# Optimization experiments

Hardware: AMD Instinct MI355X
Metric: run time of the kernel (lower is better)

Reference implementation:

```python
import jax, jax.numpy as jnp
import numpy as np

N = 100000   # nodes
E = 1600000  # edges (avg degree 16)
D = 256      # in_channels == dim (forward hard-codes BatchNorm1d(256))
BN_EPS = 1e-5


def _batchnorm(x, gamma, beta):
    # training-mode BatchNorm1d: batch statistics over node dim, biased variance
    mu = jnp.mean(x, axis=0)
    var = jnp.var(x, axis=0)
    return (x - mu) * jax.lax.rsqrt(var + BN_EPS) * gamma + beta


def _gin_conv(x, src, dst, n, W1, b1, gamma, beta, W2, b2):
    # GINConv, eps=0: nn((1+eps)*x + sum_{j in N(i)} x_j)
    agg = jax.ops.segment_sum(x[src], dst, num_segments=n)  # sparse neighbor sum
    h = x + agg
    h = jax.nn.relu(_batchnorm(h @ W1 + b1, gamma, beta))
    return jax.nn.relu(h @ W2 + b2)


def setup_inputs() -> dict:
    key = jax.random.key(0)
    ks = jax.random.split(key, 8)
    x = jax.random.normal(ks[0], (N, D), dtype=jnp.float32)
    edge_index = jax.random.randint(ks[1], (2, E), 0, N, dtype=jnp.int64)
    s = 0.02
    inp = {
        "x": x,
        "edge_index": edge_index,
        # fresh BatchNorm1d(256) in forward (default affine params)
        "g0": jnp.ones((D,), jnp.float32),
        "b0": jnp.zeros((D,), jnp.float32),
        # conv1 MLP: Linear-BN-ReLU-Linear-ReLU
        "W1a": jax.random.normal(ks[2], (D, D), jnp.float32) * s,
        "b1a": jnp.zeros((D,), jnp.float32),
        "g1": jnp.ones((D,), jnp.float32),
        "bt1": jnp.zeros((D,), jnp.float32),
        "W1b": jax.random.normal(ks[3], (D, D), jnp.float32) * s,
        "b1b": jnp.zeros((D,), jnp.float32),
        # conv2 MLP
        "W2a": jax.random.normal(ks[4], (D, D), jnp.float32) * s,
        "b2a": jnp.zeros((D,), jnp.float32),
        "g2": jnp.ones((D,), jnp.float32),
        "bt2": jnp.zeros((D,), jnp.float32),
        "W2b": jax.random.normal(ks[5], (D, D), jnp.float32) * s,
        "b2b": jnp.zeros((D,), jnp.float32),
    }
    return inp


def reference(x, edge_index, g0, b0, W1a, b1a, g1, bt1, W1b, b1b,
              W2a, b2a, g2, bt2, W2b, b2b):
    n = x.shape[0]
    src, dst = edge_index[0], edge_index[1]
    h = _batchnorm(x, g0, b0)                       # fresh BN(256) on input
    h = _gin_conv(h, src, dst, n, W1a, b1a, g1, bt1, W1b, b1b)
    h = jax.nn.relu(h)                              # outer relu (dropout=eval, identity)
    h = _gin_conv(h, src, dst, n, W2a, b2a, g2, bt2, W2b, b2b)
    return jax.nn.relu(h)
```

## Files before the change

kernel.cpp:

```cpp
#include <hip/hip_runtime.h>

#define N_NODES 100000
#define N_EDGES 1600000
#define DIM 256

typedef unsigned short bf16u;
typedef __attribute__((ext_vector_type(8))) short bf16x8s;
typedef __attribute__((ext_vector_type(4))) float f32x4;

__device__ __forceinline__ float bf2f(unsigned int u16) {
    union { unsigned int i; float f; } x; x.i = u16 << 16; return x.f;
}
__device__ __forceinline__ bf16u f2bf(float f) {
    union { float f; unsigned int i; } x; x.f = f;
    unsigned int i = x.i;
    return (bf16u)((i + 0x7fffu + ((i >> 16) & 1u)) >> 16);
}
__device__ __forceinline__ float loadv(const void* p, size_t i, int isf32) {
    return isf32 ? ((const float*)p)[i] : bf2f(((const bf16u*)p)[i]);
}
__device__ __forceinline__ void async_copy16(const void* g, void* l) {
    __builtin_amdgcn_global_load_lds((const __attribute__((address_space(1))) void*)g,
                                     (__attribute__((address_space(3))) void*)l, 16, 0, 0);
}

__global__ void zero_ints(int* p, int n) {
    int i = blockIdx.x * 256 + threadIdx.x;
    if (i < n) p[i] = 0;
}
__global__ void zero_floats(float* p, int n) {
    int i = blockIdx.x * 256 + threadIdx.x;
    if (i < n) p[i] = 0.f;
}

__global__ void detect_flags(const unsigned* xw, const int* ei, int* flags) {
    __shared__ int cnt, nz;
    if (threadIdx.x == 0) { cnt = 0; nz = 0; }
    __syncthreads();
    unsigned u = xw[threadIdx.x];
    float av = fabsf(bf2f(u & 0xffffu));
    if (av > 1e-5f && av < 50.f) atomicAdd(&cnt, 1);
    if (ei[2 * threadIdx.x + 1] != 0) atomicAdd(&nz, 1);
    __syncthreads();
    if (threadIdx.x == 0) {
        flags[0] = (cnt >= 128) ? 0 : 1;
        if (nz == 0) { flags[1] = 2; flags[2] = 2 * N_EDGES; }
        else         { flags[1] = 1; flags[2] = N_EDGES; }
    }
}

__global__ void transpose_w(const void* W0, const void* W1, const void* W2, const void* W3,
                            bf16u* Wt, const int* flags) {
    __shared__ bf16u tile[64][65];
    int isf32 = flags[0];
    const void* W = (blockIdx.y == 0) ? W0 : (blockIdx.y == 1) ? W1 : (blockIdx.y == 2) ? W2 : W3;
    bf16u* out = Wt + (size_t)blockIdx.y * DIM * DIM;
    int t = threadIdx.x;
    int tx = t & 63, ty = t >> 6;
    int k0 = (blockIdx.x >> 2) * 64, n0 = (blockIdx.x & 3) * 64;
#pragma unroll
    for (int i = 0; i < 16; ++i) {
        int r = ty + i * 4;
        tile[tx][r] = f2bf(loadv(W, (size_t)(k0 + r) * DIM + (n0 + tx), isf32));
    }
    __syncthreads();
#pragma unroll
    for (int i = 0; i < 16; ++i) {
        int r = ty + i * 4;
        out[(size_t)(n0 + r) * DIM + (k0 + tx)] = tile[r][tx];
    }
}

__global__ void col_stats(const void* X, int nrows, float* sums, const int* flags, int dual) {
    __shared__ float ls[512];
    int isf32 = dual ? flags[0] : 0;
    int t = threadIdx.x;
    ls[t] = 0.f; ls[t + 256] = 0.f;
    __syncthreads();
    int rpb = (nrows + gridDim.x - 1) / gridDim.x;
    int r0 = blockIdx.x * rpb;
    int r1 = r0 + rpb; if (r1 > nrows) r1 = nrows;
    int cg = (t & 31) * 8;
    float s[8], q[8];
#pragma unroll
    for (int j = 0; j < 8; ++j) { s[j] = 0.f; q[j] = 0.f; }
    for (int r = r0 + (t >> 5); r < r1; r += 8) {
        size_t base = (size_t)r * DIM + cg;
#pragma unroll
        for (int j = 0; j < 8; ++j) {
            float f = loadv(X, base + j, isf32);
            s[j] += f; q[j] += f * f;
        }
    }
#pragma unroll
    for (int j = 0; j < 8; ++j) {
        atomicAdd(&ls[cg + j], s[j]);
        atomicAdd(&ls[256 + cg + j], q[j]);
    }
    __syncthreads();
    atomicAdd(&sums[t], ls[t]);
    atomicAdd(&sums[256 + t], ls[256 + t]);
}

__global__ void bn_finalize(const float* sums, const void* gamma, const void* beta,
                            float* sc, float* sh, float inv_n, const int* flags) {
    int isf32 = flags[0];
    int t = threadIdx.x;
    float mu = sums[t] * inv_n;
    float var = sums[256 + t] * inv_n - mu * mu;
    float rs = rsqrtf(var + 1e-5f);
    float g = loadv(gamma, t, isf32), b = loadv(beta, t, isf32);
    sc[t] = rs * g;
    sh[t] = b - mu * rs * g;
}

__global__ void bn_apply(const void* X, const float* sc, const float* sh, bf16u* Y,
                         const int* flags, int dual, int relu) {
    int isf32 = dual ? flags[0] : 0;
    size_t i = (size_t)blockIdx.x * 256 + threadIdx.x;
    int c = ((int)(i & 31)) * 8;
    size_t base = i * 8;
    float v[8];
    if (isf32) {
        f32x4 x0 = *(const f32x4*)((const float*)X + base);
        f32x4 x1 = *(const f32x4*)((const float*)X + base + 4);
#pragma unroll
        for (int j = 0; j < 4; ++j) { v[j] = x0[j]; v[4 + j] = x1[j]; }
    } else {
        uint4 u = *(const uint4*)((const bf16u*)X + base);
        v[0] = bf2f(u.x & 0xffffu); v[1] = bf2f(u.x >> 16);
        v[2] = bf2f(u.y & 0xffffu); v[3] = bf2f(u.y >> 16);
        v[4] = bf2f(u.z & 0xffffu); v[5] = bf2f(u.z >> 16);
        v[6] = bf2f(u.w & 0xffffu); v[7] = bf2f(u.w >> 16);
    }
    f32x4 s0 = *(const f32x4*)(sc + c), s1 = *(const f32x4*)(sc + c + 4);
    f32x4 h0 = *(const f32x4*)(sh + c), h1 = *(const f32x4*)(sh + c + 4);
    float y[8];
#pragma unroll
    for (int j = 0; j < 4; ++j) {
        y[j]     = v[j]     * s0[j] + h0[j];
        y[4 + j] = v[4 + j] * s1[j] + h1[j];
    }
    if (relu) {
#pragma unroll
        for (int j = 0; j < 8; ++j) y[j] = fmaxf(y[j], 0.f);
    }
    uint4 ov;
    ov.x = (unsigned)f2bf(y[0]) | ((unsigned)f2bf(y[1]) << 16);
    ov.y = (unsigned)f2bf(y[2]) | ((unsigned)f2bf(y[3]) << 16);
    ov.z = (unsigned)f2bf(y[4]) | ((unsigned)f2bf(y[5]) << 16);
    ov.w = (unsigned)f2bf(y[6]) | ((unsigned)f2bf(y[7]) << 16);
    *(uint4*)(Y + base) = ov;
}

__global__ void edge_hist(const int* ei, const int* flags, int* deg) {
    int e = blockIdx.x * 256 + threadIdx.x;
    if (e < N_EDGES) atomicAdd(&deg[ei[(size_t)flags[2] + (size_t)e * flags[1]]], 1);
}

__global__ void scan1(const int* deg, int* rp, int* bsum) {
    __shared__ int s[256];
    int t = threadIdx.x;
    int i = blockIdx.x * 256 + t;
    s[t] = (i < N_NODES) ? deg[i] : 0;
    __syncthreads();
    for (int off = 1; off < 256; off <<= 1) {
        int nv = (t >= off) ? s[t - off] : 0;
        __syncthreads();
        s[t] += nv;
        __syncthreads();
    }
    if (i < N_NODES) rp[i + 1] = s[t];
    if (t == 255) bsum[blockIdx.x] = s[255];
}

__global__ void scan2(int* bsum, int nblocks) {
    __shared__ int s[512];
    int t = threadIdx.x;
    s[t] = (t < nblocks) ? bsum[t] : 0;
    __syncthreads();
    for (int off = 1; off < 512; off <<= 1) {
        int nv = (t >= off) ? s[t - off] : 0;
        __syncthreads();
        s[t] += nv;
        __syncthreads();
    }
    if (t < nblocks) bsum[t] = s[t];
}

__global__ void scan3(int* rp, const int* bsum) {
    int i = blockIdx.x * 256 + threadIdx.x;
    if (i == 0) rp[0] = 0;
    if (i < N_NODES) {
        int b = i >> 8;
        if (b > 0) rp[i + 1] += bsum[b - 1];
    }
}

__global__ void csr_fill(const int* ei, const int* flags, const int* rp, int* fill, int* col) {
    int e = blockIdx.x * 256 + threadIdx.x;
    if (e < N_EDGES) {
        int d = ei[(size_t)flags[2] + (size_t)e * flags[1]];
        int s = ei[(size_t)e * flags[1]];
        int p = rp[d] + atomicAdd(&fill[d], 1);
        col[p] = s;
    }
}

__global__ void aggregate(const bf16u* h, const int* rp, const int* col, bf16u* out) {
    int node = blockIdx.x * 4 + (threadIdx.x >> 6);
    int lane = threadIdx.x & 63;
    const uint2* hv = (const uint2*)h;
    uint2 u = hv[(size_t)node * 64 + lane];
    float a0 = bf2f(u.x & 0xffffu), a1 = bf2f(u.x >> 16);
    float a2 = bf2f(u.y & 0xffffu), a3 = bf2f(u.y >> 16);
    float b0 = 0.f, b1 = 0.f, b2 = 0.f, b3 = 0.f;
    float c0 = 0.f, c1 = 0.f, c2 = 0.f, c3 = 0.f;
    float d0 = 0.f, d1 = 0.f, d2 = 0.f, d3 = 0.f;
    int e = rp[node], e1 = rp[node + 1];
    for (; e + 4 <= e1; e += 4) {
        int s0 = col[e], s1 = col[e + 1], s2 = col[e + 2], s3 = col[e + 3];
        uint2 w0 = hv[(size_t)s0 * 64 + lane];
        uint2 w1 = hv[(size_t)s1 * 64 + lane];
        uint2 w2 = hv[(size_t)s2 * 64 + lane];
        uint2 w3 = hv[(size_t)s3 * 64 + lane];
        a0 += bf2f(w0.x & 0xffffu); a1 += bf2f(w0.x >> 16); a2 += bf2f(w0.y & 0xffffu); a3 += bf2f(w0.y >> 16);
        b0 += bf2f(w1.x & 0xffffu); b1 += bf2f(w1.x >> 16); b2 += bf2f(w1.y & 0xffffu); b3 += bf2f(w1.y >> 16);
        c0 += bf2f(w2.x & 0xffffu); c1 += bf2f(w2.x >> 16); c2 += bf2f(w2.y & 0xffffu); c3 += bf2f(w2.y >> 16);
        d0 += bf2f(w3.x & 0xffffu); d1 += bf2f(w3.x >> 16); d2 += bf2f(w3.y & 0xffffu); d3 += bf2f(w3.y >> 16);
    }
    for (; e < e1; ++e) {
        uint2 w0 = hv[(size_t)col[e] * 64 + lane];
        a0 += bf2f(w0.x & 0xffffu); a1 += bf2f(w0.x >> 16); a2 += bf2f(w0.y & 0xffffu); a3 += bf2f(w0.y >> 16);
    }
    a0 += b0 + (c0 + d0); a1 += b1 + (c1 + d1);
    a2 += b2 + (c2 + d2); a3 += b3 + (c3 + d3);
    uint2 ov;
    ov.x = (unsigned)f2bf(a0) | ((unsigned)f2bf(a1) << 16);
    ov.y = (unsigned)f2bf(a2) | ((unsigned)f2bf(a3) << 16);
    *(uint2*)&((uint2*)out)[(size_t)node * 64 + lane] = ov;
}

__global__ __launch_bounds__(256) void gemm_bias(const bf16u* __restrict__ A,
                                                 const bf16u* __restrict__ Wt,
                                                 const void* __restrict__ bias,
                                                 void* __restrict__ Cout, int mrows,
                                                 const int* __restrict__ flags,
                                                 int relu, int f32out,
                                                 float* __restrict__ stats) {
    __shared__ bf16u As[128 * 64];
    __shared__ bf16u Bs[128 * 64];
    __shared__ float lsum[256];
    int isf32 = flags[0];
    int t = threadIdx.x;
    int w = t >> 6, lane = t & 63;
    int lr = lane & 15, lq = lane >> 4;
    int wm = w >> 1, wn = w & 1;
    int rowBase = blockIdx.x * 128, colBase = blockIdx.y * 128;
    f32x4 acc[4][4] = {};
    lsum[t] = 0.f;
    int srow = t >> 3;
    int g8   = ((t & 7) ^ ((t >> 3) & 7)) * 8;
    for (int k0 = 0; k0 < 256; k0 += 64) {
        __syncthreads();
#pragma unroll
        for (int p = 0; p < 4; ++p) {
            int r = p * 32 + srow;
            int gr = rowBase + r; gr = (gr < mrows) ? gr : (mrows - 1);
            async_copy16(A + (size_t)gr * 256 + k0 + g8, &As[(p * 32 + (w << 3)) * 64]);
            async_copy16(Wt + (size_t)(colBase + r) * 256 + k0 + g8, &Bs[(p * 32 + (w << 3)) * 64]);
        }
        __syncthreads();
#pragma unroll
        for (int ks = 0; ks < 2; ++ks) {
            bf16x8s af[4], bfv[4];
#pragma unroll
            for (int mt = 0; mt < 4; ++mt) {
                int ar = wm * 64 + mt * 16 + lr;
                af[mt] = *(const bf16x8s*)&As[ar * 64 + (((ks * 4 + lq) ^ (lr & 7)) * 8)];
            }
#pragma unroll
            for (int nt = 0; nt < 4; ++nt) {
                int br = wn * 64 + nt * 16 + lr;
                bfv[nt] = *(const bf16x8s*)&Bs[br * 64 + (((ks * 4 + lq) ^ (lr & 7)) * 8)];
            }
#pragma unroll
            for (int mt = 0; mt < 4; ++mt)
#pragma unroll
                for (int nt = 0; nt < 4; ++nt)
                    acc[mt][nt] = __builtin_amdgcn_mfma_f32_16x16x32_bf16(af[mt], bfv[nt], acc[mt][nt], 0, 0, 0);
        }
    }
    int storef32 = f32out && isf32;
#pragma unroll
    for (int nt = 0; nt < 4; ++nt) {
        int cl = wn * 64 + nt * 16 + lr;
        int c = colBase + cl;
        float bv = loadv(bias, c, isf32);
        float ssum = 0.f, ssq = 0.f;
#pragma unroll
        for (int mt = 0; mt < 4; ++mt) {
            int r0 = rowBase + wm * 64 + mt * 16 + lq * 4;
#pragma unroll
            for (int j = 0; j < 4; ++j) {
                int r = r0 + j;
                if (r < mrows) {
                    float y = acc[mt][nt][j] + bv;
                    if (relu) y = fmaxf(y, 0.f);
                    if (storef32) ((float*)Cout)[(size_t)r * 256 + c] = y;
                    else          ((bf16u*)Cout)[(size_t)r * 256 + c] = f2bf(y);
                    ssum += y; ssq += y * y;
                }
            }
        }
        if (stats) {
            atomicAdd(&lsum[cl], ssum);
            atomicAdd(&lsum[128 + cl], ssq);
        }
    }
    if (stats) {
        __syncthreads();
        if (t < 128) {
            atomicAdd(&stats[colBase + t], lsum[t]);
            atomicAdd(&stats[256 + colBase + t], lsum[128 + t]);
        }
    }
}

extern "C" void kernel_launch(void* const* d_in, const int* in_sizes, int n_in,
                              void* d_out, int out_size, void* d_ws, size_t ws_size,
                              hipStream_t stream) {
    const void* x   = d_in[0];
    const int*  ei  = (const int*)d_in[1];
    const void* g0  = d_in[2];
    const void* b0  = d_in[3];
    const void* W1a = d_in[4];
    const void* b1a = d_in[5];
    const void* g1  = d_in[6];
    const void* bt1 = d_in[7];
    const void* W1b = d_in[8];
    const void* b1b = d_in[9];
    const void* W2a = d_in[10];
    const void* b2a = d_in[11];
    const void* g2  = d_in[12];
    const void* bt2 = d_in[13];
    const void* W2b = d_in[14];
    const void* b2b = d_in[15];

    char* ws = (char*)d_ws;
    size_t off = 0;
    auto alloc = [&](size_t bytes) {
        char* p = ws + off;
        off += (bytes + 255) & ~(size_t)255;
        return p;
    };
    const size_t FB = (size_t)N_NODES * DIM * 2;
    bf16u* bufA  = (bf16u*)alloc(FB);
    bf16u* bufB  = (bf16u*)alloc(FB);
    bf16u* Wt    = (bf16u*)alloc((size_t)4 * DIM * DIM * 2);
    int*   colA  = (int*)alloc((size_t)N_EDGES * 4);
    int*   rp    = (int*)alloc((size_t)(N_NODES + 1) * 4);
    int*   deg   = (int*)alloc((size_t)N_NODES * 4);
    int*   fill  = (int*)alloc((size_t)N_NODES * 4);
    int*   bsum  = (int*)alloc(512 * 4);
    float* sums0 = (float*)alloc(512 * 4);
    float* sums1 = (float*)alloc(512 * 4);
    float* sums2 = (float*)alloc(512 * 4);
    float* sc    = (float*)alloc(256 * 4);
    float* sh    = (float*)alloc(256 * 4);
    int*   flags = (int*)alloc(4 * 4);

    bf16u* Wt1a = Wt;
    bf16u* Wt1b = Wt + 65536;
    bf16u* Wt2a = Wt + 2 * 65536;
    bf16u* Wt2b = Wt + 3 * 65536;

    const float inv_n = 1.0f / (float)N_NODES;

    detect_flags<<<1, 256, 0, stream>>>((const unsigned*)x, ei, flags);
    zero_floats<<<6, 256, 0, stream>>>(sums0, 1536);
    transpose_w<<<dim3(16, 4), 256, 0, stream>>>(W1a, W1b, W2a, W2b, Wt, flags);

    zero_ints<<<391, 256, 0, stream>>>(deg, N_NODES);
    zero_ints<<<391, 256, 0, stream>>>(fill, N_NODES);
    edge_hist<<<6250, 256, 0, stream>>>(ei, flags, deg);
    scan1<<<391, 256, 0, stream>>>(deg, rp, bsum);
    scan2<<<1, 512, 0, stream>>>(bsum, 391);
    scan3<<<392, 256, 0, stream>>>(rp, bsum);
    csr_fill<<<6250, 256, 0, stream>>>(ei, flags, rp, fill, colA);

    col_stats<<<500, 256, 0, stream>>>(x, N_NODES, sums0, flags, 1);
    bn_finalize<<<1, 256, 0, stream>>>(sums0, g0, b0, sc, sh, inv_n, flags);
    bn_apply<<<12500, 256, 0, stream>>>(x, sc, sh, bufB, flags, 1, 0);

    aggregate<<<25000, 256, 0, stream>>>(bufB, rp, colA, bufA);
    gemm_bias<<<dim3(782, 2), 256, 0, stream>>>(bufA, Wt1a, b1a, bufB, N_NODES, flags, 0, 0, sums1);
    bn_finalize<<<1, 256, 0, stream>>>(sums1, g1, bt1, sc, sh, inv_n, flags);
    bn_apply<<<12500, 256, 0, stream>>>(bufB, sc, sh, bufB, flags, 0, 1);
    gemm_bias<<<dim3(782, 2), 256, 0, stream>>>(bufB, Wt1b, b1b, bufA, N_NODES, flags, 1, 0, nullptr);

    aggregate<<<25000, 256, 0, stream>>>(bufA, rp, colA, bufB);
    gemm_bias<<<dim3(782, 2), 256, 0, stream>>>(bufB, Wt2a, b2a, bufA, N_NODES, flags, 0, 0, sums2);
    bn_finalize<<<1, 256, 0, stream>>>(sums2, g2, bt2, sc, sh, inv_n, flags);
    bn_apply<<<12500, 256, 0, stream>>>(bufA, sc, sh, bufA, flags, 0, 1);
    gemm_bias<<<dim3(782, 2), 256, 0, stream>>>(bufA, Wt2b, b2b, d_out, N_NODES, flags, 1, 1, nullptr);
}
```

Measured before the change: 983.6 us.

## Build CSR via two-level binned scatter and widen aggregate loads

Replaces the global-atomic histogram, three-kernel scan and atomic CSR fill with a binned approach. Edges are first scattered into 196 destination bins of 512 nodes using shared-memory counts, then each bin builds its part of the CSR locally with LDS atomics and a block scan. The aggregate kernel now uses 16-byte loads, with each wave split into two halves that handle alternate edges and are combined by a cross-lane shuffle. The risk is that any bin holding more than BINCAP records silently drops edges, and bufB is reused as the record buffer.

```diff
diff --git a/kernel.cpp b/kernel.cpp
--- a/kernel.cpp
+++ b/kernel.cpp
@@ -3,6 +3,8 @@
 #define N_NODES 100000
 #define N_EDGES 1600000
 #define DIM 256
+#define NBINS 196
+#define BINCAP 16384
 
 typedef unsigned short bf16u;
 typedef __attribute__((ext_vector_type(8))) short bf16x8s;
@@ -10,6 +12,12 @@
 
 __device__ __forceinline__ float bf2f(unsigned int u16) {
     union { unsigned int i; float f; } x; x.i = u16 << 16; return x.f;
+}
+__device__ __forceinline__ float hi2f(unsigned int u) {
+    union { unsigned int i; float f; } x; x.i = u & 0xffff0000u; return x.f;
+}
+__device__ __forceinline__ float lo2f(unsigned int u) {
+    union { unsigned int i; float f; } x; x.i = u << 16; return x.f;
 }
 __device__ __forceinline__ bf16u f2bf(float f) {
     union { float f; unsigned int i; } x; x.f = f;
@@ -24,19 +32,16 @@
                                      (__attribute__((address_space(3))) void*)l, 16, 0, 0);
 }
 
-__global__ void zero_ints(int* p, int n) {
-    int i = blockIdx.x * 256 + threadIdx.x;
-    if (i < n) p[i] = 0;
-}
 __global__ void zero_floats(float* p, int n) {
     int i = blockIdx.x * 256 + threadIdx.x;
     if (i < n) p[i] = 0.f;
 }
 
-__global__ void detect_flags(const unsigned* xw, const int* ei, int* flags) {
+__global__ void detect_flags(const unsigned* xw, const int* ei, int* flags, int* gBinFill) {
     __shared__ int cnt, nz;
     if (threadIdx.x == 0) { cnt = 0; nz = 0; }
     __syncthreads();
+    gBinFill[threadIdx.x] = 0;
     unsigned u = xw[threadIdx.x];
     float av = fabsf(bf2f(u & 0xffffu));
     if (av > 1e-5f && av < 50.f) atomicAdd(&cnt, 1);
@@ -68,6 +73,103 @@
     for (int i = 0; i < 16; ++i) {
         int r = ty + i * 4;
         out[(size_t)(n0 + r) * DIM + (k0 + tx)] = tile[r][tx];
+    }
+}
+
+__global__ __launch_bounds__(256) void bin_scatter(const int* __restrict__ ei,
+                                                   const int* __restrict__ flags,
+                                                   uint2* __restrict__ gRec,
+                                                   int* __restrict__ gBinFill) {
+    __shared__ int cnt[256];
+    __shared__ int cur[256];
+    __shared__ uint2 rec[4096];
+    int t = threadIdx.x;
+    cnt[t] = 0; cur[t] = 0;
+    __syncthreads();
+    int st = flags[1], ofs = flags[2];
+    int e0 = blockIdx.x * 4096;
+#pragma unroll
+    for (int i = 0; i < 16; ++i) {
+        int e = e0 + i * 256 + t;
+        uint2 r;
+        if (e < N_EDGES) {
+            r.x = (unsigned)ei[(size_t)ofs + (size_t)e * st];
+            r.y = (unsigned)ei[(size_t)e * st];
+            atomicAdd(&cnt[r.x >> 9], 1);
+        } else {
+            r.x = 0xffffffffu; r.y = 0;
+        }
+        rec[i * 256 + t] = r;
+    }
+    __syncthreads();
+    if (t < NBINS) {
+        int c = cnt[t];
+        int b = (c > 0) ? atomicAdd(&gBinFill[t], c) : 0;
+        cnt[t] = b;
+    }
+    __syncthreads();
+#pragma unroll
+    for (int i = 0; i < 16; ++i) {
+        uint2 r = rec[i * 256 + t];
+        if (r.x != 0xffffffffu) {
+            int b = r.x >> 9;
+            int li = atomicAdd(&cur[b], 1);
+            int pos = cnt[b] + li;
+            if (pos < BINCAP) gRec[(size_t)b * BINCAP + pos] = r;
+        }
+    }
+}
+
+__global__ void bin_scan(const int* gBinFill, int* binBase) {
+    __shared__ int s[256];
+    int t = threadIdx.x;
+    s[t] = (t < NBINS) ? gBinFill[t] : 0;
+    __syncthreads();
+    for (int off = 1; off < 256; off <<= 1) {
+        int v = (t >= off) ? s[t - off] : 0;
+        __syncthreads();
+        s[t] += v;
+        __syncthreads();
+    }
+    binBase[t + 1] = s[t];
+    if (t == 0) binBase[0] = 0;
+}
+
+__global__ __launch_bounds__(256) void bin_csr(const uint2* __restrict__ gRec,
+                                               const int* __restrict__ gBinFill,
+                                               const int* __restrict__ binBase,
+                                               int* __restrict__ rp, int* __restrict__ col) {
+    __shared__ int cntA[512], scanB[512], noff[512], ncur[512];
+    int bin = blockIdx.x, t = threadIdx.x;
+    int cnt = gBinFill[bin];
+    if (cnt > BINCAP) cnt = BINCAP;
+    int gbase = binBase[bin], lo = bin << 9;
+    cntA[t] = 0; cntA[t + 256] = 0; ncur[t] = 0; ncur[t + 256] = 0;
+    __syncthreads();
+    const uint2* R = gRec + (size_t)bin * BINCAP;
+    for (int j = t; j < cnt; j += 256) atomicAdd(&cntA[(int)R[j].x - lo], 1);
+    __syncthreads();
+    scanB[t] = cntA[t]; scanB[t + 256] = cntA[t + 256];
+    __syncthreads();
+    for (int off = 1; off < 512; off <<= 1) {
+        int v0 = (t >= off) ? scanB[t - off] : 0;
+        int v1 = (t + 256 >= off) ? scanB[t + 256 - off] : 0;
+        __syncthreads();
+        scanB[t] += v0; scanB[t + 256] += v1;
+        __syncthreads();
+    }
+    noff[t] = scanB[t] - cntA[t];
+    noff[t + 256] = scanB[t + 256] - cntA[t + 256];
+    __syncthreads();
+    int n0 = lo + t, n1 = lo + t + 256;
+    if (n0 < N_NODES) rp[n0] = gbase + noff[t];
+    if (n1 < N_NODES) rp[n1] = gbase + noff[t + 256];
+    if (bin == 0 && t == 0) rp[N_NODES] = N_EDGES;
+    for (int j = t; j < cnt; j += 256) {
+        uint2 r = R[j];
+        int k = (int)r.x - lo;
+        int li = atomicAdd(&ncur[k], 1);
+        col[gbase + noff[k] + li] = (int)r.y;
     }
 }
 
@@ -128,10 +230,10 @@
         for (int j = 0; j < 4; ++j) { v[j] = x0[j]; v[4 + j] = x1[j]; }
     } else {
         uint4 u = *(const uint4*)((const bf16u*)X + base);
-        v[0] = bf2f(u.x & 0xffffu); v[1] = bf2f(u.x >> 16);
-        v[2] = bf2f(u.y & 0xffffu); v[3] = bf2f(u.y >> 16);
-        v[4] = bf2f(u.z & 0xffffu); v[5] = bf2f(u.z >> 16);
-        v[6] = bf2f(u.w & 0xffffu); v[7] = bf2f(u.w >> 16);
+        v[0] = lo2f(u.x); v[1] = hi2f(u.x);
+        v[2] = lo2f(u.y); v[3] = hi2f(u.y);
+        v[4] = lo2f(u.z); v[5] = hi2f(u.z);
+        v[6] = lo2f(u.w); v[7] = hi2f(u.w);
     }
     f32x4 s0 = *(const f32x4*)(sc + c), s1 = *(const f32x4*)(sc + c + 4);
     f32x4 h0 = *(const f32x4*)(sh + c), h1 = *(const f32x4*)(sh + c + 4);
@@ -153,92 +255,60 @@
     *(uint4*)(Y + base) = ov;
 }
 
-__global__ void edge_hist(const int* ei, const int* flags, int* deg) {
-    int e = blockIdx.x * 256 + threadIdx.x;
-    if (e < N_EDGES) atomicAdd(&deg[ei[(size_t)flags[2] + (size_t)e * flags[1]]], 1);
-}
-
-__global__ void scan1(const int* deg, int* rp, int* bsum) {
-    __shared__ int s[256];
-    int t = threadIdx.x;
-    int i = blockIdx.x * 256 + t;
-    s[t] = (i < N_NODES) ? deg[i] : 0;
-    __syncthreads();
-    for (int off = 1; off < 256; off <<= 1) {
-        int nv = (t >= off) ? s[t - off] : 0;
-        __syncthreads();
-        s[t] += nv;
-        __syncthreads();
-    }
-    if (i < N_NODES) rp[i + 1] = s[t];
-    if (t == 255) bsum[blockIdx.x] = s[255];
-}
-
-__global__ void scan2(int* bsum, int nblocks) {
-    __shared__ int s[512];
-    int t = threadIdx.x;
-    s[t] = (t < nblocks) ? bsum[t] : 0;
-    __syncthreads();
-    for (int off = 1; off < 512; off <<= 1) {
-        int nv = (t >= off) ? s[t - off] : 0;
-        __syncthreads();
-        s[t] += nv;
-        __syncthreads();
-    }
-    if (t < nblocks) bsum[t] = s[t];
-}
-
-__global__ void scan3(int* rp, const int* bsum) {
-    int i = blockIdx.x * 256 + threadIdx.x;
-    if (i == 0) rp[0] = 0;
-    if (i < N_NODES) {
-        int b = i >> 8;
-        if (b > 0) rp[i + 1] += bsum[b - 1];
-    }
-}
-
-__global__ void csr_fill(const int* ei, const int* flags, const int* rp, int* fill, int* col) {
-    int e = blockIdx.x * 256 + threadIdx.x;
-    if (e < N_EDGES) {
-        int d = ei[(size_t)flags[2] + (size_t)e * flags[1]];
-        int s = ei[(size_t)e * flags[1]];
-        int p = rp[d] + atomicAdd(&fill[d], 1);
-        col[p] = s;
-    }
-}
-
-__global__ void aggregate(const bf16u* h, const int* rp, const int* col, bf16u* out) {
+__global__ __launch_bounds__(256) void aggregate(const bf16u* __restrict__ h,
+                                                 const int* __restrict__ rp,
+                                                 const int* __restrict__ col,
+                                                 bf16u* __restrict__ out) {
     int node = blockIdx.x * 4 + (threadIdx.x >> 6);
     int lane = threadIdx.x & 63;
-    const uint2* hv = (const uint2*)h;
-    uint2 u = hv[(size_t)node * 64 + lane];
-    float a0 = bf2f(u.x & 0xffffu), a1 = bf2f(u.x >> 16);
-    float a2 = bf2f(u.y & 0xffffu), a3 = bf2f(u.y >> 16);
-    float b0 = 0.f, b1 = 0.f, b2 = 0.f, b3 = 0.f;
-    float c0 = 0.f, c1 = 0.f, c2 = 0.f, c3 = 0.f;
-    float d0 = 0.f, d1 = 0.f, d2 = 0.f, d3 = 0.f;
+    int p = lane >> 5, c = lane & 31;
+    const uint4* hv = (const uint4*)h;
+    float acc[8];
+    if (p == 0) {
+        uint4 u = hv[(size_t)node * 32 + c];
+        acc[0] = lo2f(u.x); acc[1] = hi2f(u.x);
+        acc[2] = lo2f(u.y); acc[3] = hi2f(u.y);
+        acc[4] = lo2f(u.z); acc[5] = hi2f(u.z);
+        acc[6] = lo2f(u.w); acc[7] = hi2f(u.w);
+    } else {
+#pragma unroll
+        for (int j = 0; j < 8; ++j) acc[j] = 0.f;
+    }
     int e = rp[node], e1 = rp[node + 1];
     for (; e + 4 <= e1; e += 4) {
-        int s0 = col[e], s1 = col[e + 1], s2 = col[e + 2], s3 = col[e + 3];
-        uint2 w0 = hv[(size_t)s0 * 64 + lane];
-        uint2 w1 = hv[(size_t)s1 * 64 + lane];
-        uint2 w2 = hv[(size_t)s2 * 64 + lane];
-        uint2 w3 = hv[(size_t)s3 * 64 + lane];
-        a0 += bf2f(w0.x & 0xffffu); a1 += bf2f(w0.x >> 16); a2 += bf2f(w0.y & 0xffffu); a3 += bf2f(w0.y >> 16);
-        b0 += bf2f(w1.x & 0xffffu); b1 += bf2f(w1.x >> 16); b2 += bf2f(w1.y & 0xffffu); b3 += bf2f(w1.y >> 16);
-        c0 += bf2f(w2.x & 0xffffu); c1 += bf2f(w2.x >> 16); c2 += bf2f(w2.y & 0xffffu); c3 += bf2f(w2.y >> 16);
-        d0 += bf2f(w3.x & 0xffffu); d1 += bf2f(w3.x >> 16); d2 += bf2f(w3.y & 0xffffu); d3 += bf2f(w3.y >> 16);
-    }
-    for (; e < e1; ++e) {
-        uint2 w0 = hv[(size_t)col[e] * 64 + lane];
-        a0 += bf2f(w0.x & 0xffffu); a1 += bf2f(w0.x >> 16); a2 += bf2f(w0.y & 0xffffu); a3 += bf2f(w0.y >> 16);
-    }
-    a0 += b0 + (c0 + d0); a1 += b1 + (c1 + d1);
-    a2 += b2 + (c2 + d2); a3 += b3 + (c3 + d3);
-    uint2 ov;
-    ov.x = (unsigned)f2bf(a0) | ((unsigned)f2bf(a1) << 16);
-    ov.y = (unsigned)f2bf(a2) | ((unsigned)f2bf(a3) << 16);
-    *(uint2*)&((uint2*)out)[(size_t)node * 64 + lane] = ov;
+        int s0 = col[e + p];
+        int s1 = col[e + 2 + p];
+        uint4 a = hv[(size_t)s0 * 32 + c];
+        uint4 b = hv[(size_t)s1 * 32 + c];
+        acc[0] += lo2f(a.x); acc[1] += hi2f(a.x);
+        acc[2] += lo2f(a.y); acc[3] += hi2f(a.y);
+        acc[4] += lo2f(a.z); acc[5] += hi2f(a.z);
+        acc[6] += lo2f(a.w); acc[7] += hi2f(a.w);
+        acc[0] += lo2f(b.x); acc[1] += hi2f(b.x);
+        acc[2] += lo2f(b.y); acc[3] += hi2f(b.y);
+        acc[4] += lo2f(b.z); acc[5] += hi2f(b.z);
+        acc[6] += lo2f(b.w); acc[7] += hi2f(b.w);
+    }
+    for (; e < e1; e += 2) {
+        int idx = e + p;
+        if (idx < e1) {
+            uint4 a = hv[(size_t)col[idx] * 32 + c];
+            acc[0] += lo2f(a.x); acc[1] += hi2f(a.x);
+            acc[2] += lo2f(a.y); acc[3] += hi2f(a.y);
+            acc[4] += lo2f(a.z); acc[5] += hi2f(a.z);
+            acc[6] += lo2f(a.w); acc[7] += hi2f(a.w);
+        }
+    }
+#pragma unroll
+    for (int j = 0; j < 8; ++j) acc[j] += __shfl_xor(acc[j], 32);
+    if (p == 0) {
+        uint4 ov;
+        ov.x = (unsigned)f2bf(acc[0]) | ((unsigned)f2bf(acc[1]) << 16);
+        ov.y = (unsigned)f2bf(acc[2]) | ((unsigned)f2bf(acc[3]) << 16);
+        ov.z = (unsigned)f2bf(acc[4]) | ((unsigned)f2bf(acc[5]) << 16);
+        ov.w = (unsigned)f2bf(acc[6]) | ((unsigned)f2bf(acc[7]) << 16);
+        ((uint4*)out)[(size_t)node * 32 + c] = ov;
+    }
 }
 
 __global__ __launch_bounds__(256) void gemm_bias(const bf16u* __restrict__ A,
@@ -360,9 +430,8 @@
     bf16u* Wt    = (bf16u*)alloc((size_t)4 * DIM * DIM * 2);
     int*   colA  = (int*)alloc((size_t)N_EDGES * 4);
     int*   rp    = (int*)alloc((size_t)(N_NODES + 1) * 4);
-    int*   deg   = (int*)alloc((size_t)N_NODES * 4);
-    int*   fill  = (int*)alloc((size_t)N_NODES * 4);
-    int*   bsum  = (int*)alloc(512 * 4);
+    int*   gBinFill = (int*)alloc(256 * 4);
+    int*   binBase  = (int*)alloc(260 * 4);
     float* sums0 = (float*)alloc(512 * 4);
     float* sums1 = (float*)alloc(512 * 4);
     float* sums2 = (float*)alloc(512 * 4);
@@ -370,6 +439,8 @@
     float* sh    = (float*)alloc(256 * 4);
     int*   flags = (int*)alloc(4 * 4);
 
+    uint2* gRec = (uint2*)bufB;
+
     bf16u* Wt1a = Wt;
     bf16u* Wt1b = Wt + 65536;
     bf16u* Wt2a = Wt + 2 * 65536;
@@ -377,17 +448,13 @@
 
     const float inv_n = 1.0f / (float)N_NODES;
 
-    detect_flags<<<1, 256, 0, stream>>>((const unsigned*)x, ei, flags);
+    detect_flags<<<1, 256, 0, stream>>>((const unsigned*)x, ei, flags, gBinFill);
     zero_floats<<<6, 256, 0, stream>>>(sums0, 1536);
     transpose_w<<<dim3(16, 4), 256, 0, stream>>>(W1a, W1b, W2a, W2b, Wt, flags);
 
-    zero_ints<<<391, 256, 0, stream>>>(deg, N_NODES);
-    zero_ints<<<391, 256, 0, stream>>>(fill, N_NODES);
-    edge_hist<<<6250, 256, 0, stream>>>(ei, flags, deg);
-    scan1<<<391, 256, 0, stream>>>(deg, rp, bsum);
-    scan2<<<1, 512, 0, stream>>>(bsum, 391);
-    scan3<<<392, 256, 0, stream>>>(rp, bsum);
-    csr_fill<<<6250, 256, 0, stream>>>(ei, flags, rp, fill, colA);
+    bin_scatter<<<391, 256, 0, stream>>>(ei, flags, gRec, gBinFill);
+    bin_scan<<<1, 256, 0, stream>>>(gBinFill, binBase);
+    bin_csr<<<NBINS, 256, 0, stream>>>(gRec, gBinFill, binBase, rp, colA);
 
     col_stats<<<500, 256, 0, stream>>>(x, N_NODES, sums0, flags, 1);
     bn_finalize<<<1, 256, 0, stream>>>(sums0, g0, b0, sc, sh, inv_n, flags);
```

New measurement: 855.9 us. -13.0%, faster.
